# Kernel tuning notes

Measured on AMD Instinct MI355X. Metric: run time of the kernel, lower is better.

The kernel has to match this reference:

```python
import jax, jax.numpy as jnp
import numpy as np


def setup_inputs() -> dict:
    key = jax.random.key(0)
    ks = jax.random.split(key, 8)
    B, L, D, N, DM = 2, 2048, 2048, 8, 1024
    return {
        "x": jax.random.normal(ks[0], (B, L, D), jnp.float32),
        "A_log": jax.random.normal(ks[1], (D, N), jnp.float32),
        "x_proj_w": jax.random.normal(ks[2], (2 * N, D), jnp.float32) * (D ** -0.5),
        "x_proj_b": jax.random.normal(ks[3], (2 * N,), jnp.float32) * 0.02,
        "dt_proj_w": jax.random.normal(ks[4], (D, D), jnp.float32) * (D ** -0.5),
        "dt_proj_b": jax.random.normal(ks[5], (D,), jnp.float32) * 0.02,
        "out_proj_w": jax.random.normal(ks[6], (DM, D), jnp.float32) * (D ** -0.5),
        "out_proj_b": jax.random.normal(ks[7], (DM,), jnp.float32) * 0.02,
    }


def reference(x, A_log, x_proj_w, x_proj_b, dt_proj_w, dt_proj_b, out_proj_w, out_proj_b):
    # x: (B, L, D);  A_log: (D, N)
    A = -jnp.exp(A_log)                                   # (D, N), negative -> stable decay
    x_dbl = x @ x_proj_w.T + x_proj_b                     # (B, L, 2N): per-token B_t, C_t
    Bm, Cm = jnp.split(x_dbl, 2, axis=-1)                 # each (B, L, N)
    dt = jax.nn.softplus(x @ dt_proj_w.T + dt_proj_b)     # (B, L, D) selective timestep

    Bsz, L, D = x.shape
    N = A_log.shape[1]

    def step(h, inp):
        dt_t, B_t, C_t, x_t = inp                         # (B,D),(B,N),(B,N),(B,D)
        dA = jnp.exp(dt_t[..., None] * A)                 # (B, D, N)
        dB = dt_t[..., None] * B_t[:, None, :]            # (B, D, N)
        h = dA * h + dB * x_t[..., None]                  # (B, D, N)
        y = jnp.einsum("bdn,bn->bd", h, C_t)              # (B, D)
        return h, y

    h0 = jnp.zeros((Bsz, D, N), x.dtype)
    xs = (dt.transpose(1, 0, 2), Bm.transpose(1, 0, 2),
          Cm.transpose(1, 0, 2), x.transpose(1, 0, 2))
    _, ys = jax.lax.scan(step, h0, xs)                    # ys: (L, B, D)
    y = ys.transpose(1, 0, 2)                             # (B, L, D)
    return y @ out_proj_w.T + out_proj_b                  # (B, L, d_model)
```

## Files before the change

### kernel.cpp

```cpp
#include <hip/hip_runtime.h>
#include <hip/hip_bf16.h>

constexpr int Bsz = 2;
constexpr int L   = 2048;
constexpr int D   = 2048;
constexpr int Nst = 8;
constexpr int DM  = 1024;
constexpr int M   = Bsz * L;

constexpr int CH  = 64;
constexpr int T   = L / CH;
constexpr int BDN = Bsz * D * Nst;

typedef __bf16 bf16x8 __attribute__((ext_vector_type(8)));
typedef float f32x4  __attribute__((ext_vector_type(4)));

__global__ void cvt2_f32_bf16(const float* __restrict__ a, __bf16* __restrict__ oa, int n4a,
                              const float* __restrict__ b, __bf16* __restrict__ ob, int n4b) {
    int i = blockIdx.x * blockDim.x + threadIdx.x;
    const float* src; __bf16* dst; int j;
    if (i < n4a)            { src = a; dst = oa; j = i; }
    else if (i < n4a + n4b) { src = b; dst = ob; j = i - n4a; }
    else return;
    float4 v = reinterpret_cast<const float4*>(src)[j];
    union { __bf16 bb[4]; ushort4 u; } cv;
    cv.bb[0] = (__bf16)v.x; cv.bb[1] = (__bf16)v.y; cv.bb[2] = (__bf16)v.z; cv.bb[3] = (__bf16)v.w;
    reinterpret_cast<ushort4*>(dst)[j] = cv.u;
}

__global__ __launch_bounds__(256) void xdbl_kernel(
    const float* __restrict__ x, const float* __restrict__ w,
    const float* __restrict__ bias, float* __restrict__ xdbl,
    __bf16* __restrict__ x_bf)
{
    __shared__ float sw[16 * 2048];
    const int tid = threadIdx.x;
    for (int i = tid; i < 16 * 2048 / 4; i += 256)
        reinterpret_cast<float4*>(sw)[i] = reinterpret_cast<const float4*>(w)[i];
    __syncthreads();

    const int lane = tid & 63;
    const int wrow = tid >> 6;
    for (int rr = 0; rr < 4; ++rr) {
        const int row = blockIdx.x * 16 + wrow * 4 + rr;
        const float* xr = x + (size_t)row * D;
        __bf16* xb = x_bf + (size_t)row * D;
        float acc[16];
#pragma unroll
        for (int j = 0; j < 16; ++j) acc[j] = 0.f;
        for (int k = lane * 4; k < D; k += 256) {
            float4 xv = *reinterpret_cast<const float4*>(&xr[k]);
            union { __bf16 b[4]; ushort4 u; } cv;
            cv.b[0] = (__bf16)xv.x; cv.b[1] = (__bf16)xv.y;
            cv.b[2] = (__bf16)xv.z; cv.b[3] = (__bf16)xv.w;
            *reinterpret_cast<ushort4*>(&xb[k]) = cv.u;
#pragma unroll
            for (int j = 0; j < 16; ++j) {
                float4 wv = *reinterpret_cast<const float4*>(&sw[j * D + k]);
                acc[j] += xv.x * wv.x + xv.y * wv.y + xv.z * wv.z + xv.w * wv.w;
            }
        }
#pragma unroll
        for (int j = 0; j < 16; ++j) {
            float v = acc[j];
#pragma unroll
            for (int off = 32; off > 0; off >>= 1) v += __shfl_down(v, off, 64);
            if (lane == 0) xdbl[(size_t)row * 16 + j] = v + bias[j];
        }
    }
}

__device__ inline void async16(__bf16* lds, const __bf16* g) {
    __builtin_amdgcn_global_load_lds(
        (const __attribute__((address_space(1))) void*)g,
        (__attribute__((address_space(3))) void*)lds, 16, 0, 0);
}

template <int MODE, int SWZ>
__global__ __launch_bounds__(512, 4) void gemm_bt(
    const __bf16* __restrict__ A, const __bf16* __restrict__ Bw,
    const float* __restrict__ bias, float* __restrict__ C,
    int N, int Kfull, int Ksub)
{
    constexpr int BM = 128, BN = 128, BK = 64;
    const int NT  = Ksub / BK;
    const int zoff = blockIdx.z * Ksub;
    __shared__ __attribute__((aligned(16))) __bf16 lds[2][2][BM * BK];

    int bx = blockIdx.x, by = blockIdx.y;
    if (SWZ) {
        const int lin = by * gridDim.x + bx;
        const int cpx = (gridDim.x * gridDim.y) >> 3;
        const int swz = (lin & 7) * cpx + (lin >> 3);
        bx = swz % gridDim.x; by = swz / gridDim.x;
    }

    const int tid  = threadIdx.x;
    const int lane = tid & 63;
    const int wid  = tid >> 6;
    const int wm   = wid >> 2, wn = wid & 3;
    const int rowBase = by * BM;
    const int colBase = bx * BN;
    const int lrow = lane & 15;
    const int kgrp = lane >> 4;

    float bv[2];
#pragma unroll
    for (int n = 0; n < 2; ++n)
        bv[n] = (MODE == 3) ? 0.f : bias[colBase + wn * 32 + n * 16 + lrow];
    asm volatile("s_waitcnt vmcnt(0)" ::: "memory");

    const int trow = tid >> 3;
    const int scol = ((tid & 7) ^ (trow & 7)) * 8;
    const __bf16* gA[2]; const __bf16* gB[2];
#pragma unroll
    for (int ro = 0; ro < 2; ++ro) {
        gA[ro] = A  + (size_t)(rowBase + ro * 64 + trow) * Kfull + zoff + scol;
        gB[ro] = Bw + (size_t)(colBase + ro * 64 + trow) * Kfull + zoff + scol;
    }

    f32x4 acc[4][2];
#pragma unroll
    for (int i = 0; i < 4; ++i)
#pragma unroll
        for (int j = 0; j < 2; ++j) acc[i][j] = f32x4{0.f, 0.f, 0.f, 0.f};

    auto stage = [&](int kt, int bsel) {
        const int k0 = kt * BK;
#pragma unroll
        for (int ro = 0; ro < 2; ++ro) {
            async16(&lds[bsel][0][ro * 4096 + tid * 8], gA[ro] + k0);
            async16(&lds[bsel][1][ro * 4096 + tid * 8], gB[ro] + k0);
        }
    };

    stage(0, 0);
    stage(1, 1);

    for (int t = 0; t < NT; ++t) {
        if (t == NT - 1) asm volatile("s_waitcnt vmcnt(0)" ::: "memory");
        else             asm volatile("s_waitcnt vmcnt(4)" ::: "memory");
        __builtin_amdgcn_s_barrier();

        const int cur = t & 1;
        bf16x8 af[4][2], bfr[2][2];
#pragma unroll
        for (int m = 0; m < 4; ++m) {
            const int row = wm * 64 + m * 16 + lrow;
#pragma unroll
            for (int kk = 0; kk < 2; ++kk) {
                const int slot = (kk * 4 + kgrp) ^ (lrow & 7);
                af[m][kk] = *reinterpret_cast<const bf16x8*>(&lds[cur][0][row * 64 + slot * 8]);
            }
        }
#pragma unroll
        for (int n = 0; n < 2; ++n) {
            const int row = wn * 32 + n * 16 + lrow;
#pragma unroll
            for (int kk = 0; kk < 2; ++kk) {
                const int slot = (kk * 4 + kgrp) ^ (lrow & 7);
                bfr[n][kk] = *reinterpret_cast<const bf16x8*>(&lds[cur][1][row * 64 + slot * 8]);
            }
        }
        asm volatile("s_waitcnt lgkmcnt(0)" ::: "memory");
        __builtin_amdgcn_s_barrier();

        if (t + 2 < NT) stage(t + 2, cur);

        __builtin_amdgcn_s_setprio(1);
#pragma unroll
        for (int kk = 0; kk < 2; ++kk)
#pragma unroll
            for (int m = 0; m < 4; ++m)
#pragma unroll
                for (int n = 0; n < 2; ++n)
                    acc[m][n] = __builtin_amdgcn_mfma_f32_16x16x32_bf16(af[m][kk], bfr[n][kk], acc[m][n], 0, 0, 0);
        __builtin_amdgcn_s_setprio(0);
    }

    float* Cz = (MODE == 3) ? C + (size_t)blockIdx.z * M * N : C;
#pragma unroll
    for (int m = 0; m < 4; ++m) {
        const int row = rowBase + wm * 64 + m * 16 + kgrp * 4;
#pragma unroll
        for (int n = 0; n < 2; ++n) {
            const int col = colBase + wn * 32 + n * 16 + lrow;
#pragma unroll
            for (int r = 0; r < 4; ++r) {
                float v = acc[m][n][r] + bv[n];
                if (MODE == 1) v = (v > 20.f) ? v : log1pf(expf(v));
                Cz[(size_t)(row + r) * N + col] = v;
            }
        }
    }
}

__global__ __launch_bounds__(256) void reduce_bias(
    const float* __restrict__ part, const float* __restrict__ bias,
    float* __restrict__ out)
{
    const int i = blockIdx.x * blockDim.x + threadIdx.x;
    const int n4 = M * DM / 4;
    if (i >= n4) return;
    float4 a = reinterpret_cast<const float4*>(part)[i];
    float4 b = reinterpret_cast<const float4*>(part + (size_t)M * DM)[i];
    float4 bb = *reinterpret_cast<const float4*>(&bias[(i * 4) % DM]);
    float4 r;
    r.x = a.x + b.x + bb.x; r.y = a.y + b.y + bb.y;
    r.z = a.z + b.z + bb.z; r.w = a.w + b.w + bb.w;
    reinterpret_cast<float4*>(out)[i] = r;
}

__global__ __launch_bounds__(64) void scan_p1(
    const float* __restrict__ dt, const float* __restrict__ x,
    const float* __restrict__ xdbl, const float* __restrict__ A_log,
    float* __restrict__ P, float* __restrict__ Hloc)
{
    const int tid = threadIdx.x;
    int blk = blockIdx.x;
    const int c  = blk % CH;  blk /= CH;
    const int dg = blk % (D / 64);
    const int b  = blk / (D / 64);
    const int d  = dg * 64 + tid;

    float A[Nst], h[Nst], p[Nst];
#pragma unroll
    for (int n = 0; n < Nst; ++n) {
        A[n] = -expf(A_log[(size_t)d * Nst + n]);
        h[n] = 0.f; p[n] = 1.f;
    }

    __shared__ __attribute__((aligned(16))) float sBC[T * 16];
    const float4* src = reinterpret_cast<const float4*>(xdbl + ((size_t)b * L + c * T) * 16);
#pragma unroll
    for (int i = tid; i < T * 4; i += 64)
        reinterpret_cast<float4*>(sBC)[i] = src[i];
    __syncthreads();

    const float* dt_p = dt + ((size_t)b * L + c * T) * D + d;
    const float* x_p  = x  + ((size_t)b * L + c * T) * D + d;
#pragma unroll 4
    for (int t2 = 0; t2 < T; ++t2) {
        const float dtv = dt_p[(size_t)t2 * D];
        const float xv  = x_p[(size_t)t2 * D];
        const float dtx = dtv * xv;
        const float* bc = &sBC[t2 * 16];
#pragma unroll
        for (int n = 0; n < Nst; ++n) {
            const float dA = __expf(dtv * A[n]);
            p[n] *= dA;
            h[n] = dA * h[n] + dtx * bc[n];
        }
    }
    const size_t base = ((size_t)c * Bsz * D + (size_t)b * D + d) * Nst;
#pragma unroll
    for (int n = 0; n < Nst; ++n) { P[base + n] = p[n]; Hloc[base + n] = h[n]; }
}

__global__ __launch_bounds__(256) void scan_p2(
    const float* __restrict__ P, const float* __restrict__ Hloc,
    float* __restrict__ Hstart)
{
    const int id = blockIdx.x * blockDim.x + threadIdx.x;
    if (id >= BDN) return;
    float h = 0.f;
    for (int c = 0; c < CH; ++c) {
        const size_t o = (size_t)c * BDN + id;
        Hstart[o] = h;
        h = P[o] * h + Hloc[o];
    }
}

__global__ __launch_bounds__(64) void scan_p3(
    const float* __restrict__ dt, const float* __restrict__ x,
    const float* __restrict__ xdbl, const float* __restrict__ A_log,
    const float* __restrict__ Hstart, __bf16* __restrict__ y_bf)
{
    const int tid = threadIdx.x;
    int blk = blockIdx.x;
    const int c  = blk % CH;  blk /= CH;
    const int dg = blk % (D / 64);
    const int b  = blk / (D / 64);
    const int d  = dg * 64 + tid;

    float A[Nst], h[Nst];
    const size_t hbase = ((size_t)c * Bsz * D + (size_t)b * D + d) * Nst;
#pragma unroll
    for (int n = 0; n < Nst; ++n) {
        A[n] = -expf(A_log[(size_t)d * Nst + n]);
        h[n] = Hstart[hbase + n];
    }

    __shared__ __attribute__((aligned(16))) float sBC[T * 16];
    const float4* src = reinterpret_cast<const float4*>(xdbl + ((size_t)b * L + c * T) * 16);
#pragma unroll
    for (int i = tid; i < T * 4; i += 64)
        reinterpret_cast<float4*>(sBC)[i] = src[i];
    __syncthreads();

    const float* dt_p = dt + ((size_t)b * L + c * T) * D + d;
    const float* x_p  = x  + ((size_t)b * L + c * T) * D + d;
    __bf16*      y_p  = y_bf + ((size_t)b * L + c * T) * D + d;
#pragma unroll 4
    for (int t2 = 0; t2 < T; ++t2) {
        const float dtv = dt_p[(size_t)t2 * D];
        const float xv  = x_p[(size_t)t2 * D];
        const float dtx = dtv * xv;
        const float* bc = &sBC[t2 * 16];
        float y = 0.f;
#pragma unroll
        for (int n = 0; n < Nst; ++n) {
            const float dA = __expf(dtv * A[n]);
            h[n] = dA * h[n] + dtx * bc[n];
            y = fmaf(h[n], bc[8 + n], y);
        }
        y_p[(size_t)t2 * D] = (__bf16)y;
    }
}

extern "C" void kernel_launch(void* const* d_in, const int* in_sizes, int n_in,
                              void* d_out, int out_size, void* d_ws, size_t ws_size,
                              hipStream_t stream) {
    const float* x     = (const float*)d_in[0];
    const float* A_log = (const float*)d_in[1];
    const float* xpw   = (const float*)d_in[2];
    const float* xpb   = (const float*)d_in[3];
    const float* dtw   = (const float*)d_in[4];
    const float* dtb   = (const float*)d_in[5];
    const float* ow    = (const float*)d_in[6];
    const float* ob    = (const float*)d_in[7];
    float* out = (float*)d_out;

    char* ws = (char*)d_ws;
    __bf16* x_bf   = (__bf16*)(ws);
    __bf16* dtw_bf = (__bf16*)(ws + 16777216);
    __bf16* ow_bf  = (__bf16*)(ws + 25165824);
    float*  xdbl   = (float* )(ws + 29360128);
    float*  dtbuf  = (float* )(ws + 29622272);
    __bf16* y_bf   = (__bf16*)(ws + 63176704);
    float*  P      = (float*)(ws);
    float*  Hloc   = (float*)(ws + 8388608);
    float*  Hstart = (float*)(ws + 16777216);
    float*  Cpart  = (float*)(ws + 29622272);

    const int n4a = D * D / 4, n4b = DM * D / 4;
    cvt2_f32_bf16<<<(n4a + n4b + 255) / 256, 256, 0, stream>>>(dtw, dtw_bf, n4a, ow, ow_bf, n4b);

    xdbl_kernel<<<M / 16, 256, 0, stream>>>(x, xpw, xpb, xdbl, x_bf);

    gemm_bt<1, 1><<<dim3(D / 128, M / 128, 1), 512, 0, stream>>>(x_bf, dtw_bf, dtb, dtbuf, D, D, D);

    const int scan_blocks = Bsz * (D / 64) * CH;
    scan_p1<<<scan_blocks, 64, 0, stream>>>(dtbuf, x, xdbl, A_log, P, Hloc);
    scan_p2<<<(BDN + 255) / 256, 256, 0, stream>>>(P, Hloc, Hstart);
    scan_p3<<<scan_blocks, 64, 0, stream>>>(dtbuf, x, xdbl, A_log, Hstart, y_bf);

    gemm_bt<3, 1><<<dim3(DM / 128, M / 128, 2), 512, 0, stream>>>(y_bf, ow_bf, ob, Cpart, DM, D, D / 2);
    reduce_bias<<<(M * DM / 4 + 255) / 256, 256, 0, stream>>>(Cpart, ob, out);
}
```

Measured before the change: 186.2 us.

## Store dt in bf16 and replace split-K out-proj with 64-row tile GEMM

The dt projection GEMM now writes softplus(dt) as bf16 instead of fp32, which halves the dt buffer traffic written by the GEMM and read twice by the scan passes. The output projection drops its split-K into two partial buffers plus a separate reduce_bias kernel. It now uses a new 64x128-tile GEMM that writes the biased result directly, giving 512 blocks without the partial-sum round trip. In exchange, dt loses precision and the output GEMM runs longer per block over the full K.

```diff
diff --git a/kernel.cpp b/kernel.cpp
--- a/kernel.cpp
+++ b/kernel.cpp
@@ -79,12 +79,11 @@
 template <int MODE, int SWZ>
 __global__ __launch_bounds__(512, 4) void gemm_bt(
     const __bf16* __restrict__ A, const __bf16* __restrict__ Bw,
-    const float* __restrict__ bias, float* __restrict__ C,
-    int N, int Kfull, int Ksub)
+    const float* __restrict__ bias, void* __restrict__ Cout,
+    int N, int K)
 {
     constexpr int BM = 128, BN = 128, BK = 64;
-    const int NT  = Ksub / BK;
-    const int zoff = blockIdx.z * Ksub;
+    const int NT = K / BK;
     __shared__ __attribute__((aligned(16))) __bf16 lds[2][2][BM * BK];
 
     int bx = blockIdx.x, by = blockIdx.y;
@@ -107,7 +106,7 @@
     float bv[2];
 #pragma unroll
     for (int n = 0; n < 2; ++n)
-        bv[n] = (MODE == 3) ? 0.f : bias[colBase + wn * 32 + n * 16 + lrow];
+        bv[n] = bias[colBase + wn * 32 + n * 16 + lrow];
     asm volatile("s_waitcnt vmcnt(0)" ::: "memory");
 
     const int trow = tid >> 3;
@@ -115,8 +114,8 @@
     const __bf16* gA[2]; const __bf16* gB[2];
 #pragma unroll
     for (int ro = 0; ro < 2; ++ro) {
-        gA[ro] = A  + (size_t)(rowBase + ro * 64 + trow) * Kfull + zoff + scol;
-        gB[ro] = Bw + (size_t)(colBase + ro * 64 + trow) * Kfull + zoff + scol;
+        gA[ro] = A  + (size_t)(rowBase + ro * 64 + trow) * K + scol;
+        gB[ro] = Bw + (size_t)(colBase + ro * 64 + trow) * K + scol;
     }
 
     f32x4 acc[4][2];
@@ -178,7 +177,6 @@
         __builtin_amdgcn_s_setprio(0);
     }
 
-    float* Cz = (MODE == 3) ? C + (size_t)blockIdx.z * M * N : C;
 #pragma unroll
     for (int m = 0; m < 4; ++m) {
         const int row = rowBase + wm * 64 + m * 16 + kgrp * 4;
@@ -188,31 +186,136 @@
 #pragma unroll
             for (int r = 0; r < 4; ++r) {
                 float v = acc[m][n][r] + bv[n];
-                if (MODE == 1) v = (v > 20.f) ? v : log1pf(expf(v));
-                Cz[(size_t)(row + r) * N + col] = v;
-            }
-        }
-    }
-}
-
-__global__ __launch_bounds__(256) void reduce_bias(
-    const float* __restrict__ part, const float* __restrict__ bias,
-    float* __restrict__ out)
-{
-    const int i = blockIdx.x * blockDim.x + threadIdx.x;
-    const int n4 = M * DM / 4;
-    if (i >= n4) return;
-    float4 a = reinterpret_cast<const float4*>(part)[i];
-    float4 b = reinterpret_cast<const float4*>(part + (size_t)M * DM)[i];
-    float4 bb = *reinterpret_cast<const float4*>(&bias[(i * 4) % DM]);
-    float4 r;
-    r.x = a.x + b.x + bb.x; r.y = a.y + b.y + bb.y;
-    r.z = a.z + b.z + bb.z; r.w = a.w + b.w + bb.w;
-    reinterpret_cast<float4*>(out)[i] = r;
+                if (MODE == 1) {
+                    v = (v > 20.f) ? v : log1pf(expf(v));
+                    ((__bf16*)Cout)[(size_t)(row + r) * N + col] = (__bf16)v;
+                } else {
+                    ((float*)Cout)[(size_t)(row + r) * N + col] = v;
+                }
+            }
+        }
+    }
+}
+
+template <int SWZ>
+__global__ __launch_bounds__(256, 3) void gemm_out64(
+    const __bf16* __restrict__ A, const __bf16* __restrict__ Bw,
+    const float* __restrict__ bias, float* __restrict__ C,
+    int N, int K)
+{
+    constexpr int BM = 64, BN = 128, BK = 64;
+    const int NT = K / BK;
+    __shared__ __attribute__((aligned(16))) __bf16 ldsA[2][BM * BK];
+    __shared__ __attribute__((aligned(16))) __bf16 ldsB[2][BN * BK];
+
+    int bx = blockIdx.x, by = blockIdx.y;
+    if (SWZ) {
+        const int lin = by * gridDim.x + bx;
+        const int cpx = (gridDim.x * gridDim.y) >> 3;
+        const int swz = (lin & 7) * cpx + (lin >> 3);
+        bx = swz % gridDim.x; by = swz / gridDim.x;
+    }
+
+    const int tid  = threadIdx.x;
+    const int lane = tid & 63;
+    const int wid  = tid >> 6;
+    const int wm   = wid >> 1, wn = wid & 1;
+    const int rowBase = by * BM;
+    const int colBase = bx * BN;
+    const int lrow = lane & 15;
+    const int kgrp = lane >> 4;
+
+    float bv[4];
+#pragma unroll
+    for (int n = 0; n < 4; ++n)
+        bv[n] = bias[colBase + wn * 64 + n * 16 + lrow];
+    asm volatile("s_waitcnt vmcnt(0)" ::: "memory");
+
+    const int trow = tid >> 3;
+    const int scol = ((tid & 7) ^ (trow & 7)) * 8;
+    const __bf16* gA[2]; const __bf16* gB[4];
+#pragma unroll
+    for (int ro = 0; ro < 2; ++ro)
+        gA[ro] = A + (size_t)(rowBase + ro * 32 + trow) * K + scol;
+#pragma unroll
+    for (int ro = 0; ro < 4; ++ro)
+        gB[ro] = Bw + (size_t)(colBase + ro * 32 + trow) * K + scol;
+
+    f32x4 acc[2][4];
+#pragma unroll
+    for (int i = 0; i < 2; ++i)
+#pragma unroll
+        for (int j = 0; j < 4; ++j) acc[i][j] = f32x4{0.f, 0.f, 0.f, 0.f};
+
+    auto stage = [&](int kt, int bsel) {
+        const int k0 = kt * BK;
+#pragma unroll
+        for (int ro = 0; ro < 2; ++ro)
+            async16(&ldsA[bsel][ro * 2048 + tid * 8], gA[ro] + k0);
+#pragma unroll
+        for (int ro = 0; ro < 4; ++ro)
+            async16(&ldsB[bsel][ro * 2048 + tid * 8], gB[ro] + k0);
+    };
+
+    stage(0, 0);
+    stage(1, 1);
+
+    for (int t = 0; t < NT; ++t) {
+        if (t == NT - 1) asm volatile("s_waitcnt vmcnt(0)" ::: "memory");
+        else             asm volatile("s_waitcnt vmcnt(6)" ::: "memory");
+        __builtin_amdgcn_s_barrier();
+
+        const int cur = t & 1;
+        bf16x8 af[2][2], bfr[4][2];
+#pragma unroll
+        for (int m = 0; m < 2; ++m) {
+            const int row = wm * 32 + m * 16 + lrow;
+#pragma unroll
+            for (int kk = 0; kk < 2; ++kk) {
+                const int slot = (kk * 4 + kgrp) ^ (lrow & 7);
+                af[m][kk] = *reinterpret_cast<const bf16x8*>(&ldsA[cur][row * 64 + slot * 8]);
+            }
+        }
+#pragma unroll
+        for (int n = 0; n < 4; ++n) {
+            const int row = wn * 64 + n * 16 + lrow;
+#pragma unroll
+            for (int kk = 0; kk < 2; ++kk) {
+                const int slot = (kk * 4 + kgrp) ^ (lrow & 7);
+                bfr[n][kk] = *reinterpret_cast<const bf16x8*>(&ldsB[cur][row * 64 + slot * 8]);
+            }
+        }
+        asm volatile("s_waitcnt lgkmcnt(0)" ::: "memory");
+        __builtin_amdgcn_s_barrier();
+
+        if (t + 2 < NT) stage(t + 2, cur);
+
+        __builtin_amdgcn_s_setprio(1);
+#pragma unroll
+        for (int kk = 0; kk < 2; ++kk)
+#pragma unroll
+            for (int m = 0; m < 2; ++m)
+#pragma unroll
+                for (int n = 0; n < 4; ++n)
+                    acc[m][n] = __builtin_amdgcn_mfma_f32_16x16x32_bf16(af[m][kk], bfr[n][kk], acc[m][n], 0, 0, 0);
+        __builtin_amdgcn_s_setprio(0);
+    }
+
+#pragma unroll
+    for (int m = 0; m < 2; ++m) {
+        const int row = rowBase + wm * 32 + m * 16 + kgrp * 4;
+#pragma unroll
+        for (int n = 0; n < 4; ++n) {
+            const int col = colBase + wn * 64 + n * 16 + lrow;
+#pragma unroll
+            for (int r = 0; r < 4; ++r)
+                C[(size_t)(row + r) * N + col] = acc[m][n][r] + bv[n];
+        }
+    }
 }
 
 __global__ __launch_bounds__(64) void scan_p1(
-    const float* __restrict__ dt, const float* __restrict__ x,
+    const __bf16* __restrict__ dt, const float* __restrict__ x,
     const float* __restrict__ xdbl, const float* __restrict__ A_log,
     float* __restrict__ P, float* __restrict__ Hloc)
 {
@@ -237,11 +340,11 @@
         reinterpret_cast<float4*>(sBC)[i] = src[i];
     __syncthreads();
 
-    const float* dt_p = dt + ((size_t)b * L + c * T) * D + d;
-    const float* x_p  = x  + ((size_t)b * L + c * T) * D + d;
+    const __bf16* dt_p = dt + ((size_t)b * L + c * T) * D + d;
+    const float*  x_p  = x  + ((size_t)b * L + c * T) * D + d;
 #pragma unroll 4
     for (int t2 = 0; t2 < T; ++t2) {
-        const float dtv = dt_p[(size_t)t2 * D];
+        const float dtv = (float)dt_p[(size_t)t2 * D];
         const float xv  = x_p[(size_t)t2 * D];
         const float dtx = dtv * xv;
         const float* bc = &sBC[t2 * 16];
@@ -272,7 +375,7 @@
 }
 
 __global__ __launch_bounds__(64) void scan_p3(
-    const float* __restrict__ dt, const float* __restrict__ x,
+    const __bf16* __restrict__ dt, const float* __restrict__ x,
     const float* __restrict__ xdbl, const float* __restrict__ A_log,
     const float* __restrict__ Hstart, __bf16* __restrict__ y_bf)
 {
@@ -298,12 +401,12 @@
         reinterpret_cast<float4*>(sBC)[i] = src[i];
     __syncthreads();
 
-    const float* dt_p = dt + ((size_t)b * L + c * T) * D + d;
-    const float* x_p  = x  + ((size_t)b * L + c * T) * D + d;
-    __bf16*      y_p  = y_bf + ((size_t)b * L + c * T) * D + d;
+    const __bf16* dt_p = dt + ((size_t)b * L + c * T) * D + d;
+    const float*  x_p  = x  + ((size_t)b * L + c * T) * D + d;
+    __bf16*       y_p  = y_bf + ((size_t)b * L + c * T) * D + d;
 #pragma unroll 4
     for (int t2 = 0; t2 < T; ++t2) {
-        const float dtv = dt_p[(size_t)t2 * D];
+        const float dtv = (float)dt_p[(size_t)t2 * D];
         const float xv  = x_p[(size_t)t2 * D];
         const float dtx = dtv * xv;
         const float* bc = &sBC[t2 * 16];
@@ -332,29 +435,27 @@
     float* out = (float*)d_out;
 
     char* ws = (char*)d_ws;
-    __bf16* x_bf   = (__bf16*)(ws);
-    __bf16* dtw_bf = (__bf16*)(ws + 16777216);
-    __bf16* ow_bf  = (__bf16*)(ws + 25165824);
-    float*  xdbl   = (float* )(ws + 29360128);
-    float*  dtbuf  = (float* )(ws + 29622272);
-    __bf16* y_bf   = (__bf16*)(ws + 63176704);
-    float*  P      = (float*)(ws);
-    float*  Hloc   = (float*)(ws + 8388608);
-    float*  Hstart = (float*)(ws + 16777216);
-    float*  Cpart  = (float*)(ws + 29622272);
+    __bf16* x_bf    = (__bf16*)(ws);
+    __bf16* dtw_bf  = (__bf16*)(ws + 16777216);
+    __bf16* ow_bf   = (__bf16*)(ws + 25165824);
+    float*  xdbl    = (float* )(ws + 29360128);
+    __bf16* dtbuf   = (__bf16*)(ws + 29622272);
+    __bf16* y_bf    = (__bf16*)(ws + 63176704);
+    float*  P       = (float*)(ws);
+    float*  Hloc    = (float*)(ws + 8388608);
+    float*  Hstart  = (float*)(ws + 16777216);
 
     const int n4a = D * D / 4, n4b = DM * D / 4;
     cvt2_f32_bf16<<<(n4a + n4b + 255) / 256, 256, 0, stream>>>(dtw, dtw_bf, n4a, ow, ow_bf, n4b);
 
     xdbl_kernel<<<M / 16, 256, 0, stream>>>(x, xpw, xpb, xdbl, x_bf);
 
-    gemm_bt<1, 1><<<dim3(D / 128, M / 128, 1), 512, 0, stream>>>(x_bf, dtw_bf, dtb, dtbuf, D, D, D);
+    gemm_bt<1, 1><<<dim3(D / 128, M / 128), 512, 0, stream>>>(x_bf, dtw_bf, dtb, dtbuf, D, D);
 
     const int scan_blocks = Bsz * (D / 64) * CH;
     scan_p1<<<scan_blocks, 64, 0, stream>>>(dtbuf, x, xdbl, A_log, P, Hloc);
     scan_p2<<<(BDN + 255) / 256, 256, 0, stream>>>(P, Hloc, Hstart);
     scan_p3<<<scan_blocks, 64, 0, stream>>>(dtbuf, x, xdbl, A_log, Hstart, y_bf);
 
-    gemm_bt<3, 1><<<dim3(DM / 128, M / 128, 2), 512, 0, stream>>>(y_bf, ow_bf, ob, Cpart, DM, D, D / 2);
-    reduce_bias<<<(M * DM / 4 + 255) / 256, 256, 0, stream>>>(Cpart, ob, out);
-}
+    gemm_out64<1><<<dim3(DM / 128, M / 64), 256, 0, stream>>>(y_bf, ow_bf, ob, out, DM, D);
+}
```

After: 190.4 us. +2.2%, slower.
